# Performance work log

Measured on AMD Instinct MI355X. Metric: run time of the kernel, lower is better.

## Reference

```python
import jax, jax.numpy as jnp
import numpy as np

B, C, H, W = 16, 64, 128, 128
HX, HY = 64, 64


def _rnn_scan(x, Wih, Whh, bih, bhh):
    """Vanilla tanh RNN, batch_first. x: [N, T, Cin] -> [N, T, Hh]."""
    # precompute input projection with one big GEMM
    pre = jnp.einsum('ntc,hc->nth', x, Wih) + bih + bhh  # [N,T,Hh]
    N = x.shape[0]
    h0 = jnp.zeros((N, Whh.shape[0]), dtype=x.dtype)

    def step(h, p):
        h = jnp.tanh(p + h @ Whh.T)
        return h, h

    _, ys = jax.lax.scan(step, h0, jnp.swapaxes(pre, 0, 1))  # [T,N,Hh]
    return jnp.swapaxes(ys, 0, 1)


def setup_inputs() -> dict:
    key = jax.random.key(0)
    ks = jax.random.split(key, 9)
    sx = 1.0 / np.sqrt(HX)
    sy = 1.0 / np.sqrt(HY)
    return {
        'x': jax.random.normal(ks[0], (B, C, H, W), dtype=jnp.float32),
        'Wih_x': jax.random.uniform(ks[1], (HX, C), jnp.float32, -sx, sx),
        'Whh_x': jax.random.uniform(ks[2], (HX, HX), jnp.float32, -sx, sx),
        'bih_x': jax.random.uniform(ks[3], (HX,), jnp.float32, -sx, sx),
        'bhh_x': jax.random.uniform(ks[4], (HX,), jnp.float32, -sx, sx),
        'Wih_y': jax.random.uniform(ks[5], (HY, HX), jnp.float32, -sy, sy),
        'Whh_y': jax.random.uniform(ks[6], (HY, HY), jnp.float32, -sy, sy),
        'bih_y': jax.random.uniform(ks[7], (HY,), jnp.float32, -sy, sy),
        'bhh_y': jax.random.uniform(ks[8], (HY,), jnp.float32, -sy, sy),
    }


def reference(x, Wih_x, Whh_x, bih_x, bhh_x, Wih_y, Whh_y, bih_y, bhh_y):
    b, c, h, w = x.shape
    # X-axis RNN: scan along width, sequences are rows
    xw = jnp.transpose(x, (0, 2, 3, 1)).reshape(b * h, w, c)  # [B*H, W, C]
    out_x = _rnn_scan(xw, Wih_x, Whh_x, bih_x, bhh_x)          # [B*H, W, HX]
    # Y-axis RNN: scan along height, sequences are columns
    xy = out_x.reshape(b, h, w, HX)
    xy = jnp.transpose(xy, (0, 2, 1, 3)).reshape(b * w, h, HX)  # [B*W, H, HX]
    out_y = _rnn_scan(xy, Wih_y, Whh_y, bih_y, bhh_y)           # [B*W, H, HY]
    out = out_y.reshape(b, w, h, HY)
    return jnp.transpose(out, (0, 3, 2, 1))  # [B, HY, H, W]
```

## Files before the change

kernel.cpp:

```cpp
#include <hip/hip_runtime.h>
#include <stdint.h>


#define TLEN 128
#define NSEQ 2048
#define PSH (NSEQ*64)
#define GT 16

typedef __bf16   bf16x8 __attribute__((ext_vector_type(8)));
typedef _Float16 f16x8  __attribute__((ext_vector_type(8)));
typedef _Float16 f16x4  __attribute__((ext_vector_type(4)));
typedef float    f32x4  __attribute__((ext_vector_type(4)));
typedef unsigned short u16x4 __attribute__((ext_vector_type(4)));

static __device__ __forceinline__ unsigned int fbits(float f){
    union { float f; unsigned int u; } v; v.f = f; return v.u;
}
static __device__ __forceinline__ float ubits(unsigned int u){
    union { unsigned int u; float f; } v; v.u = u; return v.f;
}
static __device__ __forceinline__ float bf2f(unsigned short s){ return ubits(((unsigned int)s) << 16); }
static __device__ __forceinline__ unsigned short f2bf(float f){
    unsigned int u = fbits(f);
    return (unsigned short)((u + 0x7FFFu + ((u >> 16) & 1u)) >> 16);
}
static __device__ __forceinline__ __bf16 us2b(unsigned short s){
    union { unsigned short u; __bf16 b; } v; v.u = s; return v.b;
}
static __device__ __forceinline__ unsigned short h2us(_Float16 h){
    union { _Float16 h; unsigned short s; } v; v.h = h; return v.s;
}
struct bfpair { __bf16 hi, lo; };
static __device__ __forceinline__ bfpair splitf(float f){
    unsigned short h = f2bf(f);
    bfpair r; r.hi = us2b(h); r.lo = us2b(f2bf(f - bf2f(h))); return r;
}
static __device__ __forceinline__ float fast_tanh(float x){
    float e = __builtin_amdgcn_exp2f(x * 2.8853900817779268f);
    return 1.0f - 2.0f * __builtin_amdgcn_rcpf(e + 1.0f);
}

__global__ __launch_bounds__(256) void k_proj0(const float* __restrict__ A,
                                               const float* __restrict__ Wih,
                                               const float* __restrict__ b1,
                                               const float* __restrict__ b2,
                                               _Float16* __restrict__ pre){
    int lane = threadIdx.x & 63;
    int wv   = threadIdx.x >> 6;
    int q    = lane >> 4, l15 = lane & 15;

    bf16x8 Whi[4][2], Wlo[4][2];
#pragma unroll
    for (int n = 0; n < 4; n++)
#pragma unroll
        for (int kc = 0; kc < 2; kc++){
            const float* p = Wih + (n * 16 + l15) * 64 + kc * 32 + q * 8;
#pragma unroll
            for (int i = 0; i < 8; i++){
                bfpair s = splitf(p[i]);
                Whi[n][kc][i] = s.hi; Wlo[n][kc][i] = s.lo;
            }
        }
    float bias[4];
#pragma unroll
    for (int n = 0; n < 4; n++){
        int j = n * 16 + l15;
        bias[n] = b1[j] + b2[j];
    }

    int row0 = blockIdx.x * 128 + wv * 32;

    float av[2][2][8];
#pragma unroll
    for (int mi = 0; mi < 2; mi++){
        int r = row0 + mi * 16 + l15;
        int b = r >> 14, hw = r & 16383;
        const float* xb = A + (size_t)b * 1048576 + hw;
#pragma unroll
        for (int kc = 0; kc < 2; kc++)
#pragma unroll
            for (int i = 0; i < 8; i++)
                av[mi][kc][i] = xb[(size_t)(kc * 32 + q * 8 + i) * 16384];
    }

#pragma unroll
    for (int mi = 0; mi < 2; mi++){
        int rb = row0 + mi * 16;
        bf16x8 Ahi[2], Alo[2];
#pragma unroll
        for (int kc = 0; kc < 2; kc++)
#pragma unroll
            for (int i = 0; i < 8; i++){
                bfpair s = splitf(av[mi][kc][i]);
                Ahi[kc][i] = s.hi; Alo[kc][i] = s.lo;
            }
        f32x4 acc[4];
#pragma unroll
        for (int n = 0; n < 4; n++) acc[n] = (f32x4){bias[n], bias[n], bias[n], bias[n]};
#pragma unroll
        for (int n = 0; n < 4; n++)
#pragma unroll
            for (int kc = 0; kc < 2; kc++){
                acc[n] = __builtin_amdgcn_mfma_f32_16x16x32_bf16(Ahi[kc], Whi[n][kc], acc[n], 0, 0, 0);
                acc[n] = __builtin_amdgcn_mfma_f32_16x16x32_bf16(Alo[kc], Whi[n][kc], acc[n], 0, 0, 0);
                acc[n] = __builtin_amdgcn_mfma_f32_16x16x32_bf16(Ahi[kc], Wlo[n][kc], acc[n], 0, 0, 0);
            }
        int bT = rb >> 14, hT = (rb >> 7) & 127, wBase = rb & 127;
        size_t seqOff = (size_t)bT * 128 + hT;
#pragma unroll
        for (int n = 0; n < 4; n++)
#pragma unroll
            for (int rr = 0; rr < 4; rr++){
                int w = wBase + q * 4 + rr;
                pre[((size_t)w * NSEQ + seqOff) * 64 + n * 16 + l15] = (_Float16)acc[n][rr];
            }
    }
}

template<int PASS>
__global__ __launch_bounds__(256) void k_scan(const _Float16* __restrict__ pre,
                                              const float* __restrict__ Whh,
                                              const float* __restrict__ Wy,
                                              const float* __restrict__ by1,
                                              const float* __restrict__ by2,
                                              _Float16* __restrict__ prey,
                                              float* __restrict__ outf){
    __shared__ alignas(16) unsigned short hbuf[2][16][64];
    int lane = threadIdx.x & 63;
    int wv   = threadIdx.x >> 6;
    int q = lane >> 4, l15 = lane & 15;
    int n0 = blockIdx.x * 16;
    int j0 = wv * 16 + q * 4;

    f16x8 Af[2];
#pragma unroll
    for (int kc = 0; kc < 2; kc++){
        const float* p = Whh + (wv * 16 + l15) * 64 + kc * 32 + q * 8;
#pragma unroll
        for (int i = 0; i < 8; i++)
            Af[kc][i] = (_Float16)p[i];
    }
    f16x8 Yf[2];
    f32x4 biasy = (f32x4){0.f, 0.f, 0.f, 0.f};
    if constexpr (PASS == 0){
#pragma unroll
        for (int kc = 0; kc < 2; kc++){
            const float* p = Wy + (wv * 16 + l15) * 64 + kc * 32 + q * 8;
#pragma unroll
            for (int i = 0; i < 8; i++)
                Yf[kc][i] = (_Float16)p[i];
        }
#pragma unroll
        for (int r = 0; r < 4; r++) biasy[r] = by1[j0 + r] + by2[j0 + r];
    }

    f16x8 Bf[2];
#pragma unroll
    for (int kc = 0; kc < 2; kc++)
#pragma unroll
        for (int i = 0; i < 8; i++) Bf[kc][i] = (_Float16)0.f;

    int bb = n0 >> 7, low7 = n0 & 127;

    const _Float16* pb = pre + (size_t)(n0 + l15) * 64 + j0;
    size_t spy = (size_t)(low7 + l15) * NSEQ + (size_t)bb * 128;

    int e   = l15 & 7;
    int wj  = (((j0 >> 3) ^ e) << 3) | (j0 & 7);
    int rj0 = ((q)     ^ e) << 3;
    int rj1 = ((4 + q) ^ e) << 3;

    f16x4 ps[GT];
    u16x4 prey_st[GT];
    f32x4 outst[GT];

    for (int g = 0; g < TLEN / GT; g++){
        int G = g * GT;
#pragma unroll
        for (int u = 0; u < GT; u++)
            ps[u] = *(const f16x4*)(pb + (size_t)(G + u) * PSH);

#pragma unroll
        for (int u = 0; u < GT; u++){
            int t = G + u;
            f32x4 a = (f32x4){(float)ps[u][0], (float)ps[u][1], (float)ps[u][2], (float)ps[u][3]};
            a = __builtin_amdgcn_mfma_f32_16x16x32_f16(Af[0], Bf[0], a, 0, 0, 0);
            a = __builtin_amdgcn_mfma_f32_16x16x32_f16(Af[1], Bf[1], a, 0, 0, 0);
            if constexpr (PASS == 0){
                f32x4 y = biasy;
                y = __builtin_amdgcn_mfma_f32_16x16x32_f16(Yf[0], Bf[0], y, 0, 0, 0);
                y = __builtin_amdgcn_mfma_f32_16x16x32_f16(Yf[1], Bf[1], y, 0, 0, 0);
#pragma unroll
                for (int r = 0; r < 4; r++)
                    prey_st[u][r] = h2us((_Float16)y[r]);
            }

            u16x4 h4;
#pragma unroll
            for (int r = 0; r < 4; r++){
                float tv = fast_tanh(a[r]);
                if constexpr (PASS == 1) outst[u][r] = tv;
                h4[r] = h2us((_Float16)tv);
            }
            int par = t & 1;
            *(u16x4*)&hbuf[par][l15][wj] = h4;
            __syncthreads();
            Bf[0] = *(const f16x8*)&hbuf[par][l15][rj0];
            Bf[1] = *(const f16x8*)&hbuf[par][l15][rj1];
        }
        if constexpr (PASS == 0){
#pragma unroll
            for (int u = 0; u < GT; u++){
                int tp = G - 1 + u;
                if (tp >= 0)
                    *(u16x4*)(prey + (spy + tp) * 64 + j0) = prey_st[u];
            }
        } else {
#pragma unroll
            for (int u = 0; u < GT; u++)
#pragma unroll
                for (int r = 0; r < 4; r++)
                    outf[((size_t)(bb * 64 + j0 + r) * TLEN + (G + u)) * 128 + low7 + l15] = outst[u][r];
        }
    }
    if constexpr (PASS == 0){
        f32x4 y = biasy;
        y = __builtin_amdgcn_mfma_f32_16x16x32_f16(Yf[0], Bf[0], y, 0, 0, 0);
        y = __builtin_amdgcn_mfma_f32_16x16x32_f16(Yf[1], Bf[1], y, 0, 0, 0);
        u16x4 pv;
#pragma unroll
        for (int r = 0; r < 4; r++)
            pv[r] = h2us((_Float16)y[r]);
        *(u16x4*)(prey + (spy + (TLEN - 1)) * 64 + j0) = pv;
    }
}

extern "C" void kernel_launch(void* const* d_in, const int* in_sizes, int n_in,
                              void* d_out, int out_size, void* d_ws, size_t ws_size,
                              hipStream_t stream){
    (void)in_sizes; (void)n_in; (void)out_size; (void)ws_size;
    const float* x    = (const float*)d_in[0];
    const float* Wihx = (const float*)d_in[1];
    const float* Whhx = (const float*)d_in[2];
    const float* bihx = (const float*)d_in[3];
    const float* bhhx = (const float*)d_in[4];
    const float* Wihy = (const float*)d_in[5];
    const float* Whhy = (const float*)d_in[6];
    const float* bihy = (const float*)d_in[7];
    const float* bhhy = (const float*)d_in[8];
    _Float16* prex = (_Float16*)d_ws;
    _Float16* prey = prex + (size_t)NSEQ * TLEN * 64;
    float* of = (float*)d_out;

    k_proj0 <<<2048, 256, 0, stream>>>(x, Wihx, bihx, bhhx, prex);
    k_scan<0><<<128, 256, 0, stream>>>(prex, Whhx, Wihy, bihy, bhhy, prey, nullptr);
    k_scan<1><<<128, 256, 0, stream>>>(prey, Whhy, nullptr, nullptr, nullptr, nullptr, of);
}
```

Measured before the change: 232.8 us.

## Run each scan block in a single wave with register-only hidden-state exchange

The recurrent scan kernels go from four waves per 16-sequence block, which traded hidden-state slices through LDS with a __syncthreads every timestep, to one wave that computes all 64 output rows. The Whh rows are permuted so the MFMA output layout of the tanh results lines up directly with the B-operand layout for the next step, so the LDS round trip and barrier disappear. Input projections are double-buffered in 4-step slabs, and outputs are stored immediately instead of batched. In exchange each step runs four times as many dependent MFMAs in one wave, and only 128 waves run in total, leaving most CUs idle and placing heavy pressure on registers.

```diff
diff --git a/kernel.cpp b/kernel.cpp
--- a/kernel.cpp
+++ b/kernel.cpp
@@ -5,7 +5,6 @@
 #define TLEN 128
 #define NSEQ 2048
 #define PSH (NSEQ*64)
-#define GT 16
 
 typedef __bf16   bf16x8 __attribute__((ext_vector_type(8)));
 typedef _Float16 f16x8  __attribute__((ext_vector_type(8)));
@@ -117,121 +116,124 @@
     }
 }
 
+
+#define JST(mt) ((((mt) & 1) * 32) + (q * 8) + (((mt) >> 1) * 4))
+
+#define LOADSLAB(PS, TBASE)                                                     \
+    _Pragma("unroll")                                                           \
+    for (int u_ = 0; u_ < 4; u_++)                                              \
+        _Pragma("unroll")                                                       \
+        for (int mt_ = 0; mt_ < 4; mt_++)                                       \
+            PS[u_][mt_] = *(const f16x4*)(pb + (size_t)((TBASE) + u_) * PSH + JST(mt_));
+
+#define STEP4(PS, TBASE)                                                        \
+    _Pragma("unroll")                                                           \
+    for (int u = 0; u < 4; u++){                                                \
+        int t = (TBASE) + u;                                                    \
+        f32x4 a[4];                                                             \
+        _Pragma("unroll")                                                       \
+        for (int mt = 0; mt < 4; mt++){                                         \
+            a[mt] = (f32x4){(float)PS[u][mt][0], (float)PS[u][mt][1],           \
+                            (float)PS[u][mt][2], (float)PS[u][mt][3]};          \
+            a[mt] = __builtin_amdgcn_mfma_f32_16x16x32_f16(Af[mt][0], Bf0, a[mt], 0, 0, 0); \
+            a[mt] = __builtin_amdgcn_mfma_f32_16x16x32_f16(Af[mt][1], Bf1, a[mt], 0, 0, 0); \
+        }                                                                       \
+        if constexpr (PASS == 0){                                               \
+            _Pragma("unroll")                                                   \
+            for (int mt = 0; mt < 4; mt++){                                     \
+                f32x4 y = biasy[mt];                                            \
+                y = __builtin_amdgcn_mfma_f32_16x16x32_f16(Yf[mt][0], Bf0, y, 0, 0, 0); \
+                y = __builtin_amdgcn_mfma_f32_16x16x32_f16(Yf[mt][1], Bf1, y, 0, 0, 0); \
+                u16x4 pv;                                                       \
+                _Pragma("unroll")                                               \
+                for (int r = 0; r < 4; r++) pv[r] = h2us((_Float16)y[r]);       \
+                if (t > 0)                                                      \
+                    *(u16x4*)(prey + (spy + (size_t)(t - 1)) * 64 + JST(mt)) = pv; \
+            }                                                                   \
+        }                                                                       \
+        f16x8 nB0, nB1;                                                         \
+        _Pragma("unroll")                                                       \
+        for (int mt = 0; mt < 4; mt++)                                          \
+            _Pragma("unroll")                                                   \
+            for (int r = 0; r < 4; r++){                                        \
+                float tv = fast_tanh(a[mt][r]);                                 \
+                if constexpr (PASS == 1)                                        \
+                    outf[((size_t)(bb * 64 + JST(mt) + r) * TLEN + t) * 128 + low7 + l15] = tv; \
+                if ((mt & 1) == 0) nB0[((mt >> 1) * 4) + r] = (_Float16)tv;     \
+                else               nB1[((mt >> 1) * 4) + r] = (_Float16)tv;     \
+            }                                                                   \
+        Bf0 = nB0; Bf1 = nB1;                                                   \
+    }
+
 template<int PASS>
-__global__ __launch_bounds__(256) void k_scan(const _Float16* __restrict__ pre,
-                                              const float* __restrict__ Whh,
-                                              const float* __restrict__ Wy,
-                                              const float* __restrict__ by1,
-                                              const float* __restrict__ by2,
-                                              _Float16* __restrict__ prey,
-                                              float* __restrict__ outf){
-    __shared__ alignas(16) unsigned short hbuf[2][16][64];
+__global__ __launch_bounds__(64) void k_scan(const _Float16* __restrict__ pre,
+                                             const float* __restrict__ Whh,
+                                             const float* __restrict__ Wy,
+                                             const float* __restrict__ by1,
+                                             const float* __restrict__ by2,
+                                             _Float16* __restrict__ prey,
+                                             float* __restrict__ outf){
     int lane = threadIdx.x & 63;
-    int wv   = threadIdx.x >> 6;
     int q = lane >> 4, l15 = lane & 15;
     int n0 = blockIdx.x * 16;
-    int j0 = wv * 16 + q * 4;
-
-    f16x8 Af[2];
-#pragma unroll
-    for (int kc = 0; kc < 2; kc++){
-        const float* p = Whh + (wv * 16 + l15) * 64 + kc * 32 + q * 8;
-#pragma unroll
-        for (int i = 0; i < 8; i++)
-            Af[kc][i] = (_Float16)p[i];
-    }
-    f16x8 Yf[2];
-    f32x4 biasy = (f32x4){0.f, 0.f, 0.f, 0.f};
+
+    f16x8 Af[4][2];
+#pragma unroll
+    for (int mt = 0; mt < 4; mt++){
+        int jrow = ((mt & 1) * 32) + ((l15 >> 2) * 8) + ((mt >> 1) * 4) + (l15 & 3);
+#pragma unroll
+        for (int kc = 0; kc < 2; kc++){
+            const float* p = Whh + jrow * 64 + kc * 32 + q * 8;
+#pragma unroll
+            for (int i = 0; i < 8; i++) Af[mt][kc][i] = (_Float16)p[i];
+        }
+    }
+    f16x8 Yf[4][2];
+    f32x4 biasy[4];
     if constexpr (PASS == 0){
 #pragma unroll
-        for (int kc = 0; kc < 2; kc++){
-            const float* p = Wy + (wv * 16 + l15) * 64 + kc * 32 + q * 8;
-#pragma unroll
-            for (int i = 0; i < 8; i++)
-                Yf[kc][i] = (_Float16)p[i];
-        }
-#pragma unroll
-        for (int r = 0; r < 4; r++) biasy[r] = by1[j0 + r] + by2[j0 + r];
-    }
-
-    f16x8 Bf[2];
-#pragma unroll
-    for (int kc = 0; kc < 2; kc++)
-#pragma unroll
-        for (int i = 0; i < 8; i++) Bf[kc][i] = (_Float16)0.f;
+        for (int mt = 0; mt < 4; mt++){
+            int jrow = ((mt & 1) * 32) + ((l15 >> 2) * 8) + ((mt >> 1) * 4) + (l15 & 3);
+#pragma unroll
+            for (int kc = 0; kc < 2; kc++){
+                const float* p = Wy + jrow * 64 + kc * 32 + q * 8;
+#pragma unroll
+                for (int i = 0; i < 8; i++) Yf[mt][kc][i] = (_Float16)p[i];
+            }
+#pragma unroll
+            for (int r = 0; r < 4; r++)
+                biasy[mt][r] = by1[JST(mt) + r] + by2[JST(mt) + r];
+        }
+    }
+
+    f16x8 Bf0, Bf1;
+#pragma unroll
+    for (int i = 0; i < 8; i++){ Bf0[i] = (_Float16)0.f; Bf1[i] = (_Float16)0.f; }
 
     int bb = n0 >> 7, low7 = n0 & 127;
 
-    const _Float16* pb = pre + (size_t)(n0 + l15) * 64 + j0;
+    const _Float16* pb = pre + (size_t)(n0 + l15) * 64;
     size_t spy = (size_t)(low7 + l15) * NSEQ + (size_t)bb * 128;
 
-    int e   = l15 & 7;
-    int wj  = (((j0 >> 3) ^ e) << 3) | (j0 & 7);
-    int rj0 = ((q)     ^ e) << 3;
-    int rj1 = ((4 + q) ^ e) << 3;
-
-    f16x4 ps[GT];
-    u16x4 prey_st[GT];
-    f32x4 outst[GT];
-
-    for (int g = 0; g < TLEN / GT; g++){
-        int G = g * GT;
-#pragma unroll
-        for (int u = 0; u < GT; u++)
-            ps[u] = *(const f16x4*)(pb + (size_t)(G + u) * PSH);
-
-#pragma unroll
-        for (int u = 0; u < GT; u++){
-            int t = G + u;
-            f32x4 a = (f32x4){(float)ps[u][0], (float)ps[u][1], (float)ps[u][2], (float)ps[u][3]};
-            a = __builtin_amdgcn_mfma_f32_16x16x32_f16(Af[0], Bf[0], a, 0, 0, 0);
-            a = __builtin_amdgcn_mfma_f32_16x16x32_f16(Af[1], Bf[1], a, 0, 0, 0);
-            if constexpr (PASS == 0){
-                f32x4 y = biasy;
-                y = __builtin_amdgcn_mfma_f32_16x16x32_f16(Yf[0], Bf[0], y, 0, 0, 0);
-                y = __builtin_amdgcn_mfma_f32_16x16x32_f16(Yf[1], Bf[1], y, 0, 0, 0);
-#pragma unroll
-                for (int r = 0; r < 4; r++)
-                    prey_st[u][r] = h2us((_Float16)y[r]);
-            }
-
-            u16x4 h4;
-#pragma unroll
-            for (int r = 0; r < 4; r++){
-                float tv = fast_tanh(a[r]);
-                if constexpr (PASS == 1) outst[u][r] = tv;
-                h4[r] = h2us((_Float16)tv);
-            }
-            int par = t & 1;
-            *(u16x4*)&hbuf[par][l15][wj] = h4;
-            __syncthreads();
-            Bf[0] = *(const f16x8*)&hbuf[par][l15][rj0];
-            Bf[1] = *(const f16x8*)&hbuf[par][l15][rj1];
-        }
-        if constexpr (PASS == 0){
-#pragma unroll
-            for (int u = 0; u < GT; u++){
-                int tp = G - 1 + u;
-                if (tp >= 0)
-                    *(u16x4*)(prey + (spy + tp) * 64 + j0) = prey_st[u];
-            }
-        } else {
-#pragma unroll
-            for (int u = 0; u < GT; u++)
-#pragma unroll
-                for (int r = 0; r < 4; r++)
-                    outf[((size_t)(bb * 64 + j0 + r) * TLEN + (G + u)) * 128 + low7 + l15] = outst[u][r];
-        }
+    f16x4 psA[4][4], psB[4][4];
+    LOADSLAB(psA, 0);
+    for (int gg = 0; gg < 16; gg++){
+        LOADSLAB(psB, gg * 8 + 4);
+        STEP4(psA, gg * 8);
+        if (gg < 15) LOADSLAB(psA, gg * 8 + 8);
+        STEP4(psB, gg * 8 + 4);
     }
     if constexpr (PASS == 0){
-        f32x4 y = biasy;
-        y = __builtin_amdgcn_mfma_f32_16x16x32_f16(Yf[0], Bf[0], y, 0, 0, 0);
-        y = __builtin_amdgcn_mfma_f32_16x16x32_f16(Yf[1], Bf[1], y, 0, 0, 0);
-        u16x4 pv;
-#pragma unroll
-        for (int r = 0; r < 4; r++)
-            pv[r] = h2us((_Float16)y[r]);
-        *(u16x4*)(prey + (spy + (TLEN - 1)) * 64 + j0) = pv;
+#pragma unroll
+        for (int mt = 0; mt < 4; mt++){
+            f32x4 y = biasy[mt];
+            y = __builtin_amdgcn_mfma_f32_16x16x32_f16(Yf[mt][0], Bf0, y, 0, 0, 0);
+            y = __builtin_amdgcn_mfma_f32_16x16x32_f16(Yf[mt][1], Bf1, y, 0, 0, 0);
+            u16x4 pv;
+#pragma unroll
+            for (int r = 0; r < 4; r++) pv[r] = h2us((_Float16)y[r]);
+            *(u16x4*)(prey + (spy + (TLEN - 1)) * 64 + JST(mt)) = pv;
+        }
     }
 }
 
@@ -253,6 +255,6 @@
     float* of = (float*)d_out;
 
     k_proj0 <<<2048, 256, 0, stream>>>(x, Wihx, bihx, bhhx, prex);
-    k_scan<0><<<128, 256, 0, stream>>>(prex, Whhx, Wihy, bihy, bhhy, prey, nullptr);
-    k_scan<1><<<128, 256, 0, stream>>>(prey, Whhy, nullptr, nullptr, nullptr, nullptr, of);
-}
+    k_scan<0><<<128, 64, 0, stream>>>(prex, Whhx, Wihy, bihy, bhhy, prey, nullptr);
+    k_scan<1><<<128, 64, 0, stream>>>(prey, Whhy, nullptr, nullptr, nullptr, nullptr, of);
+}
```

Result: slower. 261.1 us (+12.1%).

## Process two independent sequence chunks per block in RNN scan kernels

Applied to the files above, without the earlier changes.

Each scan block now handles 32 sequences as two interleaved 16-sequence chains, sharing one barrier per timestep and giving each wave two independent MFMA/tanh dependency chains to overlap. The grid is halved to 64 blocks and the prefetch group size drops to 8 to limit register pressure. The aim is to hide the serial recurrence latency and amortize barrier cost. The trade-off is that only 64 blocks now run on a GPU with far more compute units, and register use rises.

```diff
diff --git a/kernel.cpp b/kernel.cpp
--- a/kernel.cpp
+++ b/kernel.cpp
@@ -5,7 +5,7 @@
 #define TLEN 128
 #define NSEQ 2048
 #define PSH (NSEQ*64)
-#define GT 16
+#define GT 8
 
 typedef __bf16   bf16x8 __attribute__((ext_vector_type(8)));
 typedef _Float16 f16x8  __attribute__((ext_vector_type(8)));
@@ -125,11 +125,11 @@
                                               const float* __restrict__ by2,
                                               _Float16* __restrict__ prey,
                                               float* __restrict__ outf){
-    __shared__ alignas(16) unsigned short hbuf[2][16][64];
+    __shared__ alignas(16) unsigned short hbuf[2][2][16][64];
     int lane = threadIdx.x & 63;
     int wv   = threadIdx.x >> 6;
     int q = lane >> 4, l15 = lane & 15;
-    int n0 = blockIdx.x * 16;
+    int n0 = blockIdx.x * 32;
     int j0 = wv * 16 + q * 4;
 
     f16x8 Af[2];
@@ -154,84 +154,107 @@
         for (int r = 0; r < 4; r++) biasy[r] = by1[j0 + r] + by2[j0 + r];
     }
 
-    f16x8 Bf[2];
-#pragma unroll
-    for (int kc = 0; kc < 2; kc++)
-#pragma unroll
-        for (int i = 0; i < 8; i++) Bf[kc][i] = (_Float16)0.f;
+    f16x8 Bf[2][2];
+#pragma unroll
+    for (int c = 0; c < 2; c++)
+#pragma unroll
+        for (int kc = 0; kc < 2; kc++)
+#pragma unroll
+            for (int i = 0; i < 8; i++) Bf[c][kc][i] = (_Float16)0.f;
 
     int bb = n0 >> 7, low7 = n0 & 127;
 
-    const _Float16* pb = pre + (size_t)(n0 + l15) * 64 + j0;
-    size_t spy = (size_t)(low7 + l15) * NSEQ + (size_t)bb * 128;
+    const _Float16* pb[2];
+    size_t spy[2];
+#pragma unroll
+    for (int c = 0; c < 2; c++){
+        pb[c]  = pre + (size_t)(n0 + c * 16 + l15) * 64 + j0;
+        spy[c] = (size_t)(low7 + c * 16 + l15) * NSEQ + (size_t)bb * 128;
+    }
 
     int e   = l15 & 7;
     int wj  = (((j0 >> 3) ^ e) << 3) | (j0 & 7);
     int rj0 = ((q)     ^ e) << 3;
     int rj1 = ((4 + q) ^ e) << 3;
 
-    f16x4 ps[GT];
-    u16x4 prey_st[GT];
-    f32x4 outst[GT];
+    f16x4 ps[2][GT];
+    u16x4 prey_st[2][GT];
+    f32x4 outst[2][GT];
 
     for (int g = 0; g < TLEN / GT; g++){
         int G = g * GT;
 #pragma unroll
-        for (int u = 0; u < GT; u++)
-            ps[u] = *(const f16x4*)(pb + (size_t)(G + u) * PSH);
+        for (int c = 0; c < 2; c++)
+#pragma unroll
+            for (int u = 0; u < GT; u++)
+                ps[c][u] = *(const f16x4*)(pb[c] + (size_t)(G + u) * PSH);
 
 #pragma unroll
         for (int u = 0; u < GT; u++){
             int t = G + u;
-            f32x4 a = (f32x4){(float)ps[u][0], (float)ps[u][1], (float)ps[u][2], (float)ps[u][3]};
-            a = __builtin_amdgcn_mfma_f32_16x16x32_f16(Af[0], Bf[0], a, 0, 0, 0);
-            a = __builtin_amdgcn_mfma_f32_16x16x32_f16(Af[1], Bf[1], a, 0, 0, 0);
-            if constexpr (PASS == 0){
-                f32x4 y = biasy;
-                y = __builtin_amdgcn_mfma_f32_16x16x32_f16(Yf[0], Bf[0], y, 0, 0, 0);
-                y = __builtin_amdgcn_mfma_f32_16x16x32_f16(Yf[1], Bf[1], y, 0, 0, 0);
-#pragma unroll
-                for (int r = 0; r < 4; r++)
-                    prey_st[u][r] = h2us((_Float16)y[r]);
-            }
-
-            u16x4 h4;
-#pragma unroll
-            for (int r = 0; r < 4; r++){
-                float tv = fast_tanh(a[r]);
-                if constexpr (PASS == 1) outst[u][r] = tv;
-                h4[r] = h2us((_Float16)tv);
-            }
             int par = t & 1;
-            *(u16x4*)&hbuf[par][l15][wj] = h4;
+#pragma unroll
+            for (int c = 0; c < 2; c++){
+                f32x4 a = (f32x4){(float)ps[c][u][0], (float)ps[c][u][1],
+                                  (float)ps[c][u][2], (float)ps[c][u][3]};
+                a = __builtin_amdgcn_mfma_f32_16x16x32_f16(Af[0], Bf[c][0], a, 0, 0, 0);
+                a = __builtin_amdgcn_mfma_f32_16x16x32_f16(Af[1], Bf[c][1], a, 0, 0, 0);
+                if constexpr (PASS == 0){
+                    f32x4 y = biasy;
+                    y = __builtin_amdgcn_mfma_f32_16x16x32_f16(Yf[0], Bf[c][0], y, 0, 0, 0);
+                    y = __builtin_amdgcn_mfma_f32_16x16x32_f16(Yf[1], Bf[c][1], y, 0, 0, 0);
+#pragma unroll
+                    for (int r = 0; r < 4; r++)
+                        prey_st[c][u][r] = h2us((_Float16)y[r]);
+                }
+                u16x4 h4;
+#pragma unroll
+                for (int r = 0; r < 4; r++){
+                    float tv = fast_tanh(a[r]);
+                    if constexpr (PASS == 1) outst[c][u][r] = tv;
+                    h4[r] = h2us((_Float16)tv);
+                }
+                *(u16x4*)&hbuf[c][par][l15][wj] = h4;
+            }
             __syncthreads();
-            Bf[0] = *(const f16x8*)&hbuf[par][l15][rj0];
-            Bf[1] = *(const f16x8*)&hbuf[par][l15][rj1];
+#pragma unroll
+            for (int c = 0; c < 2; c++){
+                Bf[c][0] = *(const f16x8*)&hbuf[c][par][l15][rj0];
+                Bf[c][1] = *(const f16x8*)&hbuf[c][par][l15][rj1];
+            }
         }
         if constexpr (PASS == 0){
 #pragma unroll
-            for (int u = 0; u < GT; u++){
-                int tp = G - 1 + u;
-                if (tp >= 0)
-                    *(u16x4*)(prey + (spy + tp) * 64 + j0) = prey_st[u];
-            }
+            for (int c = 0; c < 2; c++)
+#pragma unroll
+                for (int u = 0; u < GT; u++){
+                    int tp = G - 1 + u;
+                    if (tp >= 0)
+                        *(u16x4*)(prey + (spy[c] + tp) * 64 + j0) = prey_st[c][u];
+                }
         } else {
 #pragma unroll
-            for (int u = 0; u < GT; u++)
-#pragma unroll
-                for (int r = 0; r < 4; r++)
-                    outf[((size_t)(bb * 64 + j0 + r) * TLEN + (G + u)) * 128 + low7 + l15] = outst[u][r];
+            for (int c = 0; c < 2; c++)
+#pragma unroll
+                for (int u = 0; u < GT; u++)
+#pragma unroll
+                    for (int r = 0; r < 4; r++)
+                        outf[((size_t)(bb * 64 + j0 + r) * TLEN + (G + u)) * 128
+                             + low7 + c * 16 + l15] = outst[c][u][r];
         }
     }
     if constexpr (PASS == 0){
-        f32x4 y = biasy;
-        y = __builtin_amdgcn_mfma_f32_16x16x32_f16(Yf[0], Bf[0], y, 0, 0, 0);
-        y = __builtin_amdgcn_mfma_f32_16x16x32_f16(Yf[1], Bf[1], y, 0, 0, 0);
-        u16x4 pv;
-#pragma unroll
-        for (int r = 0; r < 4; r++)
-            pv[r] = h2us((_Float16)y[r]);
-        *(u16x4*)(prey + (spy + (TLEN - 1)) * 64 + j0) = pv;
+#pragma unroll
+        for (int c = 0; c < 2; c++){
+            f32x4 y = biasy;
+            y = __builtin_amdgcn_mfma_f32_16x16x32_f16(Yf[0], Bf[c][0], y, 0, 0, 0);
+            y = __builtin_amdgcn_mfma_f32_16x16x32_f16(Yf[1], Bf[c][1], y, 0, 0, 0);
+            u16x4 pv;
+#pragma unroll
+            for (int r = 0; r < 4; r++)
+                pv[r] = h2us((_Float16)y[r]);
+            *(u16x4*)(prey + (spy[c] + (TLEN - 1)) * 64 + j0) = pv;
+        }
     }
 }
 
@@ -253,6 +276,6 @@
     float* of = (float*)d_out;
 
     k_proj0 <<<2048, 256, 0, stream>>>(x, Wihx, bihx, bhhx, prex);
-    k_scan<0><<<128, 256, 0, stream>>>(prex, Whhx, Wihy, bihy, bhhy, prey, nullptr);
-    k_scan<1><<<128, 256, 0, stream>>>(prey, Whhy, nullptr, nullptr, nullptr, nullptr, of);
-}
+    k_scan<0><<<64, 256, 0, stream>>>(prex, Whhx, Wihy, bihy, bhhy, prey, nullptr);
+    k_scan<1><<<64, 256, 0, stream>>>(prey, Whhy, nullptr, nullptr, nullptr, nullptr, of);
+}
```

Result: slower. 312.9 us (+34.4%).
